# Performance work log

Hardware: AMD Instinct MI355X
Metric: run time of the kernel (lower is better)

## Reference

```python
import jax, jax.numpy as jnp
import numpy as np

N = 50000          # nodes
E_RAND = 800000    # random edges (avg degree 16); self-loops appended per PyG GATConv default
IN = 128
HID = 32
HEADS = 4
OUT = 32
NEG_SLOPE = 0.2    # PyG GATConv default LeakyReLU slope


def setup_inputs() -> dict:
    key = jax.random.key(0)
    ks = jax.random.split(key, 8)
    x = jax.random.normal(ks[0], (N, IN), dtype=jnp.float32)
    src = jax.random.randint(ks[1], (E_RAND,), 0, N)
    dst = jax.random.randint(ks[2], (E_RAND,), 0, N)
    loops = jnp.arange(N)
    src = jnp.concatenate([src, loops])  # [E] with self-loops
    dst = jnp.concatenate([dst, loops])
    inp = {"x": x, "src": src, "dst": dst}
    layer_dims = [(IN, HID), (HID * HEADS, HID), (HID * HEADS, OUT)]
    for l, (din, c) in enumerate(layer_dims):
        k1, k2, k3 = jax.random.split(ks[3 + l], 3)
        s = 1.0 / np.sqrt(din)
        inp[f"W{l}"] = jax.random.uniform(k1, (HEADS * c, din), jnp.float32, -s, s)
        inp[f"asrc{l}"] = jax.random.uniform(k2, (HEADS, c), jnp.float32, -s, s)
        inp[f"adst{l}"] = jax.random.uniform(k3, (HEADS, c), jnp.float32, -s, s)
        inp[f"b{l}"] = jnp.zeros((HEADS * c,), jnp.float32)
    return inp


def _gat_conv(x, src, dst, W, a_src, a_dst, b):
    H, C = a_src.shape
    h = (x @ W.T).reshape(-1, H, C)                     # [N, H, C]
    al_s = jnp.einsum('nhc,hc->nh', h, a_src)           # node-level src score
    al_d = jnp.einsum('nhc,hc->nh', h, a_dst)           # node-level dst score
    e = jax.nn.leaky_relu(al_s[src] + al_d[dst], NEG_SLOPE)  # [E, H]
    # segment softmax over edges sharing the same destination node
    e_max = jax.ops.segment_max(e, dst, num_segments=N)
    e = jnp.exp(e - e_max[dst])
    denom = jax.ops.segment_sum(e, dst, num_segments=N)
    alpha = e / (denom[dst] + 1e-16)                    # [E, H]
    out = jax.ops.segment_sum(alpha[:, :, None] * h[src], dst, num_segments=N)  # [N, H, C]
    return out.reshape(-1, H * C) + b


def reference(x, src, dst, W0, asrc0, adst0, b0, W1, asrc1, adst1, b1, W2, asrc2, adst2, b2):
    params = [(W0, asrc0, adst0, b0), (W1, asrc1, adst1, b1), (W2, asrc2, adst2, b2)]
    h = x
    for i, (W, a_s, a_d, b) in enumerate(params):
        h = _gat_conv(h, src, dst, W, a_s, a_d, b)
        if i != len(params) - 1:
            h = jax.nn.elu(h)  # dropout p=0.5 is identity in eval mode
    return h
```

## Files before the change

kernel.cpp:

```cpp
#include <hip/hip_runtime.h>
#include <stdint.h>

typedef unsigned short ushort_t;
typedef unsigned int uint32;

typedef __attribute__((ext_vector_type(8))) short short8;
typedef __attribute__((ext_vector_type(4))) float floatx4;

#define NEG_SLOPE 0.2f

__device__ __forceinline__ ushort_t f2bf(float f) {
    union { float f; uint32 u; } v; v.f = f;
    uint32 u = v.u;
    uint32 r = (u + 0x7fffu + ((u >> 16) & 1u)) >> 16;
    return (ushort_t)r;
}
__device__ __forceinline__ float2 bf2x(uint32 u) {
    union { uint32 u; float f; } a, b;
    a.u = u << 16; b.u = u & 0xffff0000u;
    float2 r; r.x = a.f; r.y = b.f; return r;
}

__global__ void k_sniff(const uint32* __restrict__ x, int* __restrict__ flag) {
    __shared__ int sh[256];
    int t = threadIdx.x;
    int c = 0;
    for (int i = t; i < 1024; i += 256) {
        uint32 h = x[i] & 0xFFFFu;
        uint32 e = (h >> 7) & 0xFFu;
        if (h == 0u || (e >= 100u && e <= 140u)) c++;
    }
    sh[t] = c; __syncthreads();
    for (int off = 128; off >= 1; off >>= 1) {
        if (t < off) sh[t] += sh[t + off];
        __syncthreads();
    }
    if (t == 0) flag[0] = (sh[0] >= 512) ? 1 : 0;
}

__global__ void k_canon_params(const void* W0, const void* W1, const void* W2,
                               const void* s0, const void* s1, const void* s2,
                               const void* a0, const void* a1, const void* a2,
                               const void* b0, const void* b1, const void* b2,
                               ushort_t* __restrict__ dst, const int* __restrict__ flag) {
    int i = blockIdx.x * 256 + threadIdx.x;
    if (i >= 50304) return;
    const void* src; int off;
    if (i < 49152) {
        int seg = i / 16384; off = i % 16384;
        src = seg == 0 ? W0 : seg == 1 ? W1 : W2;
    } else if (i < 49536) {
        int j = i - 49152; int seg = j / 128; off = j % 128;
        src = seg == 0 ? s0 : seg == 1 ? s1 : s2;
    } else if (i < 49920) {
        int j = i - 49536; int seg = j / 128; off = j % 128;
        src = seg == 0 ? a0 : seg == 1 ? a1 : a2;
    } else {
        int j = i - 49920; int seg = j / 128; off = j % 128;
        src = seg == 0 ? b0 : seg == 1 ? b1 : b2;
    }
    if (flag[0]) dst[i] = ((const ushort_t*)src)[off];
    else         dst[i] = f2bf(((const float*)src)[off]);
}

__global__ void k_hist(const int* __restrict__ dst, int* __restrict__ cnt,
                       int* __restrict__ rank, int E) {
    int e = blockIdx.x * 256 + threadIdx.x;
    if (e < E) rank[e] = atomicAdd(&cnt[dst[e]], 1);
}

__global__ void k_scan_a(const int* __restrict__ cnt, int* __restrict__ ro,
                         int* __restrict__ bsum, int n) {
    __shared__ int sd[256];
    int t = threadIdx.x;
    int base = blockIdx.x * 1024 + t * 4;
    int v0 = (base + 0 < n) ? cnt[base + 0] : 0;
    int v1 = (base + 1 < n) ? cnt[base + 1] : 0;
    int v2 = (base + 2 < n) ? cnt[base + 2] : 0;
    int v3 = (base + 3 < n) ? cnt[base + 3] : 0;
    int s = v0 + v1 + v2 + v3;
    sd[t] = s; __syncthreads();
    for (int off = 1; off < 256; off <<= 1) {
        int x = 0;
        if (t >= off) x = sd[t - off];
        __syncthreads();
        sd[t] += x;
        __syncthreads();
    }
    int run = sd[t] - s;
    run += v0; if (base + 0 < n) ro[base + 1] = run;
    run += v1; if (base + 1 < n) ro[base + 2] = run;
    run += v2; if (base + 2 < n) ro[base + 3] = run;
    run += v3; if (base + 3 < n) ro[base + 4] = run;
    if (t == 255) bsum[blockIdx.x] = sd[255];
}

__global__ void k_scan_bc(int* __restrict__ ro, const int* __restrict__ bsum,
                          int n, int nb) {
    __shared__ int pre[256];
    int t = threadIdx.x;
    if (t == 0) {
        int acc = 0;
        for (int b = 0; b < nb; b++) { pre[b] = acc; acc += bsum[b]; }
    }
    __syncthreads();
    int i = blockIdx.x * 256 + t;
    if (i == 0) ro[0] = 0;
    if (i < n) ro[i + 1] += pre[i >> 10];
}

__global__ void k_scatter(const int* __restrict__ src, const int* __restrict__ dst,
                          const int* __restrict__ ro, const int* __restrict__ rank,
                          int* __restrict__ ssrc, int E) {
    int e = blockIdx.x * 256 + threadIdx.x;
    if (e < E) {
        int d = dst[e];
        ssrc[ro[d] + rank[e]] = src[e] << 8;
    }
}

__global__ __launch_bounds__(256) void k_gemm(const void* __restrict__ actv,
                                              const ushort_t* __restrict__ W,
                                              ushort_t* __restrict__ hb,
                                              float* __restrict__ als,
                                              float* __restrict__ ald,
                                              const ushort_t* __restrict__ asrcp,
                                              const ushort_t* __restrict__ adstp,
                                              int N, int layer0,
                                              const int* __restrict__ flag) {
    int wid = threadIdx.x >> 6, lane = threadIdx.x & 63;
    int n0 = (blockIdx.x * 4 + wid) * 16;
    int mrow = lane & 15, quad = lane >> 4;
    int n = n0 + mrow;
    bool isf32 = (layer0 && !flag[0]);
    short8 a[4];
    if (n < N) {
        if (isf32) {
            const float* ar = (const float*)actv + (size_t)n * 128 + quad * 8;
            #pragma unroll
            for (int kt = 0; kt < 4; kt++) {
                float4 fa = *(const float4*)(ar + kt * 32);
                float4 fb = *(const float4*)(ar + kt * 32 + 4);
                short8 v;
                v[0] = (short)f2bf(fa.x); v[1] = (short)f2bf(fa.y);
                v[2] = (short)f2bf(fa.z); v[3] = (short)f2bf(fa.w);
                v[4] = (short)f2bf(fb.x); v[5] = (short)f2bf(fb.y);
                v[6] = (short)f2bf(fb.z); v[7] = (short)f2bf(fb.w);
                a[kt] = v;
            }
        } else {
            const ushort_t* ar = (const ushort_t*)actv + (size_t)n * 128 + quad * 8;
            #pragma unroll
            for (int kt = 0; kt < 4; kt++) a[kt] = *(const short8*)(ar + kt * 32);
        }
    } else {
        #pragma unroll
        for (int kt = 0; kt < 4; kt++) { short8 z = {0,0,0,0,0,0,0,0}; a[kt] = z; }
    }
    float ps[4], pd[4];
    #pragma unroll
    for (int t = 0; t < 8; t++) {
        if ((t & 1) == 0) {
            #pragma unroll
            for (int r = 0; r < 4; r++) { ps[r] = 0.f; pd[r] = 0.f; }
        }
        const ushort_t* wr = W + (size_t)(t * 16 + mrow) * 128 + quad * 8;
        floatx4 acc = {0.f, 0.f, 0.f, 0.f};
        #pragma unroll
        for (int kt = 0; kt < 4; kt++) {
            short8 b = *(const short8*)(wr + kt * 32);
            acc = __builtin_amdgcn_mfma_f32_16x16x32_bf16(a[kt], b, acc, 0, 0, 0);
        }
        int col = t * 16 + mrow;
        union { uint32 u; float f; } cs, cd;
        cs.u = ((uint32)asrcp[col]) << 16;
        cd.u = ((uint32)adstp[col]) << 16;
        #pragma unroll
        for (int r = 0; r < 4; r++) {
            int rn = n0 + quad * 4 + r;
            if (rn < N) hb[(size_t)rn * 128 + col] = f2bf(acc[r]);
            ps[r] += acc[r] * cs.f;
            pd[r] += acc[r] * cd.f;
        }
        if (t & 1) {
            #pragma unroll
            for (int off = 1; off <= 8; off <<= 1) {
                #pragma unroll
                for (int r = 0; r < 4; r++) {
                    ps[r] += __shfl_xor(ps[r], off);
                    pd[r] += __shfl_xor(pd[r], off);
                }
            }
            int h = t >> 1;
            if (mrow < 8) {
                int r = mrow & 3;
                float vs = r == 0 ? ps[0] : r == 1 ? ps[1] : r == 2 ? ps[2] : ps[3];
                float vd = r == 0 ? pd[0] : r == 1 ? pd[1] : r == 2 ? pd[2] : pd[3];
                int rn = n0 + quad * 4 + r;
                if (rn < N) {
                    float* dp = (mrow < 4) ? als : ald;
                    dp[(size_t)rn * 4 + h] = (mrow < 4) ? vs : vd;
                }
            }
        }
    }
}

__global__ __launch_bounds__(128) void k_agg(const int* __restrict__ ro, const int* __restrict__ ssrc,
                                             const ushort_t* __restrict__ hb,
                                             const float* __restrict__ als, const float* __restrict__ ald_,
                                             const ushort_t* __restrict__ bias,
                                             void* __restrict__ outp, int N, int apply_elu,
                                             int is_final, const int* __restrict__ flag) {
    __shared__ __align__(16) float tsm_all[2][1024];
    __shared__ int osm_all[2][256];
    int wv = threadIdx.x >> 6, lane = threadIdx.x & 63;
    int n = blockIdx.x * 2 + wv;
    if (n >= N) return;
    float* tsm = tsm_all[wv];
    int* osm = osm_all[wv];
    int r0 = ro[n], r1 = ro[n + 1];
    int deg = r1 - r0;
    int degc = deg < 256 ? deg : 256;
    floatx4 ad = *(const floatx4*)(ald_ + (size_t)n * 4);
    const char* alsb = (const char*)als;

    float m0 = -1e30f, m1 = -1e30f, m2 = -1e30f, m3 = -1e30f;
    for (int e = lane; e < degc; e += 64) {
        int off = ssrc[r0 + e];
        osm[e] = off;
        floatx4 as = *(const floatx4*)(alsb + (off >> 4));
        float t0 = as.x + ad.x; t0 = t0 > 0.f ? t0 : NEG_SLOPE * t0; m0 = fmaxf(m0, t0);
        float t1 = as.y + ad.y; t1 = t1 > 0.f ? t1 : NEG_SLOPE * t1; m1 = fmaxf(m1, t1);
        float t2 = as.z + ad.z; t2 = t2 > 0.f ? t2 : NEG_SLOPE * t2; m2 = fmaxf(m2, t2);
        float t3 = as.w + ad.w; t3 = t3 > 0.f ? t3 : NEG_SLOPE * t3; m3 = fmaxf(m3, t3);
        floatx4 t4 = {t0, t1, t2, t3};
        *(floatx4*)(tsm + e * 4) = t4;
    }
    for (int i = r0 + 256 + lane; i < r1; i += 64) {
        int off = ssrc[i];
        floatx4 as = *(const floatx4*)(alsb + (off >> 4));
        float t0 = as.x + ad.x; t0 = t0 > 0.f ? t0 : NEG_SLOPE * t0; m0 = fmaxf(m0, t0);
        float t1 = as.y + ad.y; t1 = t1 > 0.f ? t1 : NEG_SLOPE * t1; m1 = fmaxf(m1, t1);
        float t2 = as.z + ad.z; t2 = t2 > 0.f ? t2 : NEG_SLOPE * t2; m2 = fmaxf(m2, t2);
        float t3 = as.w + ad.w; t3 = t3 > 0.f ? t3 : NEG_SLOPE * t3; m3 = fmaxf(m3, t3);
    }
    #pragma unroll
    for (int off = 32; off >= 1; off >>= 1) {
        m0 = fmaxf(m0, __shfl_xor(m0, off));
        m1 = fmaxf(m1, __shfl_xor(m1, off));
        m2 = fmaxf(m2, __shfl_xor(m2, off));
        m3 = fmaxf(m3, __shfl_xor(m3, off));
    }

    float d0 = 0.f, d1 = 0.f, d2 = 0.f, d3 = 0.f;
    __builtin_amdgcn_wave_barrier();
    for (int e = lane; e < degc; e += 64) {
        floatx4 t4 = *(const floatx4*)(tsm + e * 4);
        float w0 = __expf(t4.x - m0); d0 += w0;
        float w1 = __expf(t4.y - m1); d1 += w1;
        float w2 = __expf(t4.z - m2); d2 += w2;
        float w3 = __expf(t4.w - m3); d3 += w3;
        floatx4 w4 = {w0, w1, w2, w3};
        *(floatx4*)(tsm + e * 4) = w4;
    }
    __builtin_amdgcn_wave_barrier();

    int hd = lane >> 4;
    const char* hbase = (const char*)hb + (lane << 2);
    float a0 = 0.f, a1 = 0.f;
    int j = 0;
    for (; j + 2 <= degc; j += 2) {
        float wa = tsm[j * 4 + hd];
        float wb = tsm[j * 4 + 4 + hd];
        int oa = osm[j], ob = osm[j + 1];
        uint32 ha = *(const uint32*)(hbase + oa);
        uint32 hc = *(const uint32*)(hbase + ob);
        float2 pa = bf2x(ha), pb = bf2x(hc);
        a0 += wa * pa.x; a1 += wa * pa.y;
        a0 += wb * pb.x; a1 += wb * pb.y;
    }
    if (j < degc) {
        float wa = tsm[j * 4 + hd];
        int oa = osm[j];
        uint32 ha = *(const uint32*)(hbase + oa);
        float2 pa = bf2x(ha);
        a0 += wa * pa.x; a1 += wa * pa.y;
    }
    for (int i2 = r0 + 256; i2 < r1; i2++) {
        int off = ssrc[i2];
        floatx4 as = *(const floatx4*)(alsb + (off >> 4));
        float t0 = as.x + ad.x; t0 = t0 > 0.f ? t0 : NEG_SLOPE * t0; float w0 = __expf(t0 - m0);
        float t1 = as.y + ad.y; t1 = t1 > 0.f ? t1 : NEG_SLOPE * t1; float w1 = __expf(t1 - m1);
        float t2 = as.z + ad.z; t2 = t2 > 0.f ? t2 : NEG_SLOPE * t2; float w2 = __expf(t2 - m2);
        float t3 = as.w + ad.w; t3 = t3 > 0.f ? t3 : NEG_SLOPE * t3; float w3 = __expf(t3 - m3);
        if (lane == 0) { d0 += w0; d1 += w1; d2 += w2; d3 += w3; }
        float wsel = hd == 0 ? w0 : hd == 1 ? w1 : hd == 2 ? w2 : w3;
        uint32 ha = *(const uint32*)(hbase + off);
        float2 pa = bf2x(ha);
        a0 += wsel * pa.x; a1 += wsel * pa.y;
    }

    #pragma unroll
    for (int off = 32; off >= 1; off >>= 1) {
        d0 += __shfl_xor(d0, off); d1 += __shfl_xor(d1, off);
        d2 += __shfl_xor(d2, off); d3 += __shfl_xor(d3, off);
    }
    float den = (hd == 0 ? d0 : hd == 1 ? d1 : hd == 2 ? d2 : d3) + 1e-16f;
    float inv = 1.0f / den;
    int c0 = lane * 2;
    float2 bv = bf2x(*(const uint32*)(bias + c0));
    float o0 = a0 * inv + bv.x;
    float o1 = a1 * inv + bv.y;
    if (apply_elu) {
        o0 = o0 > 0.f ? o0 : expm1f(o0);
        o1 = o1 > 0.f ? o1 : expm1f(o1);
    }
    if (is_final && !flag[0]) {
        float2 o; o.x = o0; o.y = o1;
        *(float2*)((float*)outp + (size_t)n * 128 + c0) = o;
    } else {
        uint32 pack = (uint32)f2bf(o0) | ((uint32)f2bf(o1) << 16);
        *(uint32*)((ushort_t*)outp + (size_t)n * 128 + c0) = pack;
    }
}

extern "C" void kernel_launch(void* const* d_in, const int* in_sizes, int n_in,
                              void* d_out, int out_size, void* d_ws, size_t ws_size,
                              hipStream_t stream) {
    const void* x = d_in[0];
    const int* src = (const int*)d_in[1];
    const int* dst = (const int*)d_in[2];
    const int N = in_sizes[0] / 128;
    const int E = in_sizes[1];

    char* p = (char*)d_ws;
    auto alloc = [&](size_t bytes) { char* r = p; p += (bytes + 255) & ~(size_t)255; return r; };
    int*      flag  = (int*)alloc(256);
    int*      ro    = (int*)alloc((size_t)(N + 1) * 4);
    int*      ssrc  = (int*)alloc((size_t)E * 4);
    ushort_t* hb    = (ushort_t*)alloc((size_t)N * 128 * 2);
    float*    als   = (float*)alloc((size_t)N * 4 * 4);
    float*    ald   = (float*)alloc((size_t)N * 4 * 4);
    ushort_t* xact  = (ushort_t*)alloc((size_t)N * 128 * 2);
    ushort_t* pblk  = (ushort_t*)alloc((size_t)50304 * 2);

    int* cnt  = (int*)hb;
    int* bsum = (int*)((char*)hb + (size_t)N * 4);
    int* rank = (int*)xact;

    int g256e = (E + 255) / 256;
    int g256n = (N + 255) / 256;
    int nb = (N + 1023) / 1024;

    k_sniff<<<1, 256, 0, stream>>>((const uint32*)x, flag);
    k_canon_params<<<(50304 + 255) / 256, 256, 0, stream>>>(
        d_in[3], d_in[7], d_in[11],
        d_in[4], d_in[8], d_in[12],
        d_in[5], d_in[9], d_in[13],
        d_in[6], d_in[10], d_in[14],
        pblk, flag);

    hipMemsetAsync(cnt, 0, (size_t)N * 4, stream);
    k_hist<<<g256e, 256, 0, stream>>>(dst, cnt, rank, E);
    k_scan_a<<<nb, 256, 0, stream>>>(cnt, ro, bsum, N);
    k_scan_bc<<<g256n, 256, 0, stream>>>(ro, bsum, N, nb);
    k_scatter<<<g256e, 256, 0, stream>>>(src, dst, ro, rank, ssrc, E);

    int gg = (N + 63) / 64;
    int ga = (N + 1) / 2;
    const void* actin = x;
    for (int l = 0; l < 3; l++) {
        const ushort_t* Wc = pblk + (size_t)l * 16384;
        const ushort_t* As = pblk + 49152 + l * 128;
        const ushort_t* Ad = pblk + 49536 + l * 128;
        const ushort_t* Bc = pblk + 49920 + l * 128;
        void* outp = (l == 2) ? d_out : (void*)xact;
        k_gemm<<<gg, 256, 0, stream>>>(actin, Wc, hb, als, ald, As, Ad, N, l == 0 ? 1 : 0, flag);
        k_agg<<<ga, 128, 0, stream>>>(ro, ssrc, hb, als, ald, Bc, outp, N, l < 2 ? 1 : 0,
                                      l == 2 ? 1 : 0, flag);
        actin = xact;
    }
}
```

Baseline: 382.2 us.

## Fuse setup launches, use 16-bit edge indices, restructure aggregation per wave

Merges parameter canonicalisation with the degree histogram, and the first scan pass with the layer-0 GEMM, so independent work shares one launch. Sorted source indices are now stored as 16-bit values, halving index traffic; this only works while the node count fits in 16 bits. The aggregation kernel now runs one wavefront per node and processes edges in chunks of 64, staging weights and offsets in shared memory. This removes the 256-edge cap and its serial fallback loop, at the cost of recomputing the attention scores in the second pass.

```diff
diff --git a/kernel.cpp b/kernel.cpp
--- a/kernel.cpp
+++ b/kernel.cpp
@@ -38,98 +38,18 @@
     if (t == 0) flag[0] = (sh[0] >= 512) ? 1 : 0;
 }
 
-__global__ void k_canon_params(const void* W0, const void* W1, const void* W2,
-                               const void* s0, const void* s1, const void* s2,
-                               const void* a0, const void* a1, const void* a2,
-                               const void* b0, const void* b1, const void* b2,
-                               ushort_t* __restrict__ dst, const int* __restrict__ flag) {
-    int i = blockIdx.x * 256 + threadIdx.x;
-    if (i >= 50304) return;
-    const void* src; int off;
-    if (i < 49152) {
-        int seg = i / 16384; off = i % 16384;
-        src = seg == 0 ? W0 : seg == 1 ? W1 : W2;
-    } else if (i < 49536) {
-        int j = i - 49152; int seg = j / 128; off = j % 128;
-        src = seg == 0 ? s0 : seg == 1 ? s1 : s2;
-    } else if (i < 49920) {
-        int j = i - 49536; int seg = j / 128; off = j % 128;
-        src = seg == 0 ? a0 : seg == 1 ? a1 : a2;
-    } else {
-        int j = i - 49920; int seg = j / 128; off = j % 128;
-        src = seg == 0 ? b0 : seg == 1 ? b1 : b2;
-    }
-    if (flag[0]) dst[i] = ((const ushort_t*)src)[off];
-    else         dst[i] = f2bf(((const float*)src)[off]);
-}
-
-__global__ void k_hist(const int* __restrict__ dst, int* __restrict__ cnt,
-                       int* __restrict__ rank, int E) {
-    int e = blockIdx.x * 256 + threadIdx.x;
-    if (e < E) rank[e] = atomicAdd(&cnt[dst[e]], 1);
-}
-
-__global__ void k_scan_a(const int* __restrict__ cnt, int* __restrict__ ro,
-                         int* __restrict__ bsum, int n) {
-    __shared__ int sd[256];
-    int t = threadIdx.x;
-    int base = blockIdx.x * 1024 + t * 4;
-    int v0 = (base + 0 < n) ? cnt[base + 0] : 0;
-    int v1 = (base + 1 < n) ? cnt[base + 1] : 0;
-    int v2 = (base + 2 < n) ? cnt[base + 2] : 0;
-    int v3 = (base + 3 < n) ? cnt[base + 3] : 0;
-    int s = v0 + v1 + v2 + v3;
-    sd[t] = s; __syncthreads();
-    for (int off = 1; off < 256; off <<= 1) {
-        int x = 0;
-        if (t >= off) x = sd[t - off];
-        __syncthreads();
-        sd[t] += x;
-        __syncthreads();
-    }
-    int run = sd[t] - s;
-    run += v0; if (base + 0 < n) ro[base + 1] = run;
-    run += v1; if (base + 1 < n) ro[base + 2] = run;
-    run += v2; if (base + 2 < n) ro[base + 3] = run;
-    run += v3; if (base + 3 < n) ro[base + 4] = run;
-    if (t == 255) bsum[blockIdx.x] = sd[255];
-}
-
-__global__ void k_scan_bc(int* __restrict__ ro, const int* __restrict__ bsum,
-                          int n, int nb) {
-    __shared__ int pre[256];
-    int t = threadIdx.x;
-    if (t == 0) {
-        int acc = 0;
-        for (int b = 0; b < nb; b++) { pre[b] = acc; acc += bsum[b]; }
-    }
-    __syncthreads();
-    int i = blockIdx.x * 256 + t;
-    if (i == 0) ro[0] = 0;
-    if (i < n) ro[i + 1] += pre[i >> 10];
-}
-
-__global__ void k_scatter(const int* __restrict__ src, const int* __restrict__ dst,
-                          const int* __restrict__ ro, const int* __restrict__ rank,
-                          int* __restrict__ ssrc, int E) {
-    int e = blockIdx.x * 256 + threadIdx.x;
-    if (e < E) {
-        int d = dst[e];
-        ssrc[ro[d] + rank[e]] = src[e] << 8;
-    }
-}
-
-__global__ __launch_bounds__(256) void k_gemm(const void* __restrict__ actv,
-                                              const ushort_t* __restrict__ W,
-                                              ushort_t* __restrict__ hb,
-                                              float* __restrict__ als,
-                                              float* __restrict__ ald,
-                                              const ushort_t* __restrict__ asrcp,
-                                              const ushort_t* __restrict__ adstp,
-                                              int N, int layer0,
-                                              const int* __restrict__ flag) {
-    int wid = threadIdx.x >> 6, lane = threadIdx.x & 63;
-    int n0 = (blockIdx.x * 4 + wid) * 16;
+__device__ __forceinline__ void gemm_body(int bid, int tid,
+                                          const void* __restrict__ actv,
+                                          const ushort_t* __restrict__ W,
+                                          ushort_t* __restrict__ hb,
+                                          float* __restrict__ als,
+                                          float* __restrict__ ald,
+                                          const ushort_t* __restrict__ asrcp,
+                                          const ushort_t* __restrict__ adstp,
+                                          int N, int layer0,
+                                          const int* __restrict__ flag) {
+    int wid = tid >> 6, lane = tid & 63;
+    int n0 = (bid * 4 + wid) * 16;
     int mrow = lane & 15, quad = lane >> 4;
     int n = n0 + mrow;
     bool isf32 = (layer0 && !flag[0]);
@@ -206,40 +126,128 @@
     }
 }
 
-__global__ __launch_bounds__(128) void k_agg(const int* __restrict__ ro, const int* __restrict__ ssrc,
-                                             const ushort_t* __restrict__ hb,
-                                             const float* __restrict__ als, const float* __restrict__ ald_,
-                                             const ushort_t* __restrict__ bias,
-                                             void* __restrict__ outp, int N, int apply_elu,
-                                             int is_final, const int* __restrict__ flag) {
-    __shared__ __align__(16) float tsm_all[2][1024];
-    __shared__ int osm_all[2][256];
-    int wv = threadIdx.x >> 6, lane = threadIdx.x & 63;
-    int n = blockIdx.x * 2 + wv;
-    if (n >= N) return;
-    float* tsm = tsm_all[wv];
-    int* osm = osm_all[wv];
+__global__ __launch_bounds__(256) void k_gemm(const void* __restrict__ actv,
+                                              const ushort_t* __restrict__ W,
+                                              ushort_t* __restrict__ hb,
+                                              float* __restrict__ als,
+                                              float* __restrict__ ald,
+                                              const ushort_t* __restrict__ asrcp,
+                                              const ushort_t* __restrict__ adstp,
+                                              int N, const int* __restrict__ flag) {
+    gemm_body(blockIdx.x, threadIdx.x, actv, W, hb, als, ald, asrcp, adstp, N, 0, flag);
+}
+
+__global__ void k_f1(const void* W0, const void* W1, const void* W2,
+                     const void* s0, const void* s1, const void* s2,
+                     const void* a0, const void* a1, const void* a2,
+                     const void* b0, const void* b1, const void* b2,
+                     ushort_t* __restrict__ pblk, const int* __restrict__ flag,
+                     const int* __restrict__ dst, int* __restrict__ cnt,
+                     int* __restrict__ rank, int E) {
+    if (blockIdx.x < 197) {
+        int i = blockIdx.x * 256 + threadIdx.x;
+        if (i >= 50304) return;
+        const void* src; int off;
+        if (i < 49152) {
+            int seg = i / 16384; off = i % 16384;
+            src = seg == 0 ? W0 : seg == 1 ? W1 : W2;
+        } else if (i < 49536) {
+            int j = i - 49152; int seg = j / 128; off = j % 128;
+            src = seg == 0 ? s0 : seg == 1 ? s1 : s2;
+        } else if (i < 49920) {
+            int j = i - 49536; int seg = j / 128; off = j % 128;
+            src = seg == 0 ? a0 : seg == 1 ? a1 : a2;
+        } else {
+            int j = i - 49920; int seg = j / 128; off = j % 128;
+            src = seg == 0 ? b0 : seg == 1 ? b1 : b2;
+        }
+        if (flag[0]) pblk[i] = ((const ushort_t*)src)[off];
+        else         pblk[i] = f2bf(((const float*)src)[off]);
+    } else {
+        int e = (blockIdx.x - 197) * 256 + threadIdx.x;
+        if (e < E) rank[e] = atomicAdd(&cnt[dst[e]], 1);
+    }
+}
+
+__global__ __launch_bounds__(256) void k_f2(const int* __restrict__ cnt, int* __restrict__ ro,
+                                            int* __restrict__ bsum, int n, int nb,
+                                            const void* __restrict__ actv,
+                                            const ushort_t* __restrict__ W,
+                                            ushort_t* __restrict__ hb,
+                                            float* __restrict__ als, float* __restrict__ ald,
+                                            const ushort_t* __restrict__ asrcp,
+                                            const ushort_t* __restrict__ adstp,
+                                            int N, const int* __restrict__ flag) {
+    if ((int)blockIdx.x < nb) {
+        __shared__ int sd[256];
+        int t = threadIdx.x;
+        int base = blockIdx.x * 1024 + t * 4;
+        int v0 = (base + 0 < n) ? cnt[base + 0] : 0;
+        int v1 = (base + 1 < n) ? cnt[base + 1] : 0;
+        int v2 = (base + 2 < n) ? cnt[base + 2] : 0;
+        int v3 = (base + 3 < n) ? cnt[base + 3] : 0;
+        int s = v0 + v1 + v2 + v3;
+        sd[t] = s; __syncthreads();
+        for (int off = 1; off < 256; off <<= 1) {
+            int x = 0;
+            if (t >= off) x = sd[t - off];
+            __syncthreads();
+            sd[t] += x;
+            __syncthreads();
+        }
+        int run = sd[t] - s;
+        run += v0; if (base + 0 < n) ro[base + 1] = run;
+        run += v1; if (base + 1 < n) ro[base + 2] = run;
+        run += v2; if (base + 2 < n) ro[base + 3] = run;
+        run += v3; if (base + 3 < n) ro[base + 4] = run;
+        if (t == 255) bsum[blockIdx.x] = sd[255];
+    } else {
+        gemm_body(blockIdx.x - nb, threadIdx.x, actv, W, hb, als, ald, asrcp, adstp, N, 1, flag);
+    }
+}
+
+__global__ void k_scan_bc(int* __restrict__ ro, const int* __restrict__ bsum,
+                          int n, int nb) {
+    __shared__ int pre[256];
+    int t = threadIdx.x;
+    if (t == 0) {
+        int acc = 0;
+        for (int b = 0; b < nb; b++) { pre[b] = acc; acc += bsum[b]; }
+    }
+    __syncthreads();
+    int i = blockIdx.x * 256 + t;
+    if (i == 0) ro[0] = 0;
+    if (i < n) ro[i + 1] += pre[i >> 10];
+}
+
+__global__ void k_scatter(const int* __restrict__ src, const int* __restrict__ dst,
+                          const int* __restrict__ ro, const int* __restrict__ rank,
+                          ushort_t* __restrict__ ssrc, int E) {
+    int e = blockIdx.x * 256 + threadIdx.x;
+    if (e < E) {
+        int d = dst[e];
+        ssrc[ro[d] + rank[e]] = (ushort_t)src[e];
+    }
+}
+
+__global__ __launch_bounds__(64) void k_agg(const int* __restrict__ ro,
+                                            const ushort_t* __restrict__ ssrc,
+                                            const ushort_t* __restrict__ hb,
+                                            const float* __restrict__ als,
+                                            const float* __restrict__ ald_,
+                                            const ushort_t* __restrict__ bias,
+                                            void* __restrict__ outp, int N, int apply_elu,
+                                            int is_final, const int* __restrict__ flag) {
+    int n = blockIdx.x;
+    int lane = threadIdx.x;
     int r0 = ro[n], r1 = ro[n + 1];
-    int deg = r1 - r0;
-    int degc = deg < 256 ? deg : 256;
     floatx4 ad = *(const floatx4*)(ald_ + (size_t)n * 4);
     const char* alsb = (const char*)als;
 
     float m0 = -1e30f, m1 = -1e30f, m2 = -1e30f, m3 = -1e30f;
-    for (int e = lane; e < degc; e += 64) {
-        int off = ssrc[r0 + e];
-        osm[e] = off;
-        floatx4 as = *(const floatx4*)(alsb + (off >> 4));
-        float t0 = as.x + ad.x; t0 = t0 > 0.f ? t0 : NEG_SLOPE * t0; m0 = fmaxf(m0, t0);
-        float t1 = as.y + ad.y; t1 = t1 > 0.f ? t1 : NEG_SLOPE * t1; m1 = fmaxf(m1, t1);
-        float t2 = as.z + ad.z; t2 = t2 > 0.f ? t2 : NEG_SLOPE * t2; m2 = fmaxf(m2, t2);
-        float t3 = as.w + ad.w; t3 = t3 > 0.f ? t3 : NEG_SLOPE * t3; m3 = fmaxf(m3, t3);
-        floatx4 t4 = {t0, t1, t2, t3};
-        *(floatx4*)(tsm + e * 4) = t4;
-    }
-    for (int i = r0 + 256 + lane; i < r1; i += 64) {
-        int off = ssrc[i];
-        floatx4 as = *(const floatx4*)(alsb + (off >> 4));
+    for (int i = r0 + lane; i < r1; i += 64) {
+        int s = ssrc[i];
+        floatx4 as = *(const floatx4*)(alsb + (s << 4));
         float t0 = as.x + ad.x; t0 = t0 > 0.f ? t0 : NEG_SLOPE * t0; m0 = fmaxf(m0, t0);
         float t1 = as.y + ad.y; t1 = t1 > 0.f ? t1 : NEG_SLOPE * t1; m1 = fmaxf(m1, t1);
         float t2 = as.z + ad.z; t2 = t2 > 0.f ? t2 : NEG_SLOPE * t2; m2 = fmaxf(m2, t2);
@@ -253,54 +261,37 @@
         m3 = fmaxf(m3, __shfl_xor(m3, off));
     }
 
+    __shared__ __align__(16) float wsm[256];
+    __shared__ int osm[64];
+    float a0 = 0.f, a1 = 0.f;
     float d0 = 0.f, d1 = 0.f, d2 = 0.f, d3 = 0.f;
-    __builtin_amdgcn_wave_barrier();
-    for (int e = lane; e < degc; e += 64) {
-        floatx4 t4 = *(const floatx4*)(tsm + e * 4);
-        float w0 = __expf(t4.x - m0); d0 += w0;
-        float w1 = __expf(t4.y - m1); d1 += w1;
-        float w2 = __expf(t4.z - m2); d2 += w2;
-        float w3 = __expf(t4.w - m3); d3 += w3;
-        floatx4 w4 = {w0, w1, w2, w3};
-        *(floatx4*)(tsm + e * 4) = w4;
-    }
-    __builtin_amdgcn_wave_barrier();
-
     int hd = lane >> 4;
-    const char* hbase = (const char*)hb + (lane << 2);
-    float a0 = 0.f, a1 = 0.f;
-    int j = 0;
-    for (; j + 2 <= degc; j += 2) {
-        float wa = tsm[j * 4 + hd];
-        float wb = tsm[j * 4 + 4 + hd];
-        int oa = osm[j], ob = osm[j + 1];
-        uint32 ha = *(const uint32*)(hbase + oa);
-        uint32 hc = *(const uint32*)(hbase + ob);
-        float2 pa = bf2x(ha), pb = bf2x(hc);
-        a0 += wa * pa.x; a1 += wa * pa.y;
-        a0 += wb * pb.x; a1 += wb * pb.y;
-    }
-    if (j < degc) {
-        float wa = tsm[j * 4 + hd];
-        int oa = osm[j];
-        uint32 ha = *(const uint32*)(hbase + oa);
-        float2 pa = bf2x(ha);
-        a0 += wa * pa.x; a1 += wa * pa.y;
-    }
-    for (int i2 = r0 + 256; i2 < r1; i2++) {
-        int off = ssrc[i2];
-        floatx4 as = *(const floatx4*)(alsb + (off >> 4));
-        float t0 = as.x + ad.x; t0 = t0 > 0.f ? t0 : NEG_SLOPE * t0; float w0 = __expf(t0 - m0);
-        float t1 = as.y + ad.y; t1 = t1 > 0.f ? t1 : NEG_SLOPE * t1; float w1 = __expf(t1 - m1);
-        float t2 = as.z + ad.z; t2 = t2 > 0.f ? t2 : NEG_SLOPE * t2; float w2 = __expf(t2 - m2);
-        float t3 = as.w + ad.w; t3 = t3 > 0.f ? t3 : NEG_SLOPE * t3; float w3 = __expf(t3 - m3);
-        if (lane == 0) { d0 += w0; d1 += w1; d2 += w2; d3 += w3; }
-        float wsel = hd == 0 ? w0 : hd == 1 ? w1 : hd == 2 ? w2 : w3;
-        uint32 ha = *(const uint32*)(hbase + off);
-        float2 pa = bf2x(ha);
-        a0 += wsel * pa.x; a1 += wsel * pa.y;
-    }
-
+    int laneb = lane << 2;
+    for (int base = r0; base < r1; base += 64) {
+        int i = base + lane;
+        if (i < r1) {
+            int s = ssrc[i];
+            floatx4 as = *(const floatx4*)(alsb + (s << 4));
+            float t0 = as.x + ad.x; t0 = t0 > 0.f ? t0 : NEG_SLOPE * t0; float w0 = __expf(t0 - m0); d0 += w0;
+            float t1 = as.y + ad.y; t1 = t1 > 0.f ? t1 : NEG_SLOPE * t1; float w1 = __expf(t1 - m1); d1 += w1;
+            float t2 = as.z + ad.z; t2 = t2 > 0.f ? t2 : NEG_SLOPE * t2; float w2 = __expf(t2 - m2); d2 += w2;
+            float t3 = as.w + ad.w; t3 = t3 > 0.f ? t3 : NEG_SLOPE * t3; float w3 = __expf(t3 - m3); d3 += w3;
+            osm[lane] = s << 8;
+            floatx4 w4 = {w0, w1, w2, w3};
+            *(floatx4*)(wsm + lane * 4) = w4;
+        }
+        __builtin_amdgcn_wave_barrier();
+        int cend = min(64, r1 - base);
+        #pragma unroll 4
+        for (int j = 0; j < cend; j++) {
+            float wj = wsm[j * 4 + hd];
+            uint32 h2 = *(const uint32*)((const char*)hb + (uint32)(osm[j] + laneb));
+            float2 p = bf2x(h2);
+            a0 += wj * p.x;
+            a1 += wj * p.y;
+        }
+        __builtin_amdgcn_wave_barrier();
+    }
     #pragma unroll
     for (int off = 32; off >= 1; off >>= 1) {
         d0 += __shfl_xor(d0, off); d1 += __shfl_xor(d1, off);
@@ -337,48 +328,46 @@
     char* p = (char*)d_ws;
     auto alloc = [&](size_t bytes) { char* r = p; p += (bytes + 255) & ~(size_t)255; return r; };
     int*      flag  = (int*)alloc(256);
+    int*      bsum  = (int*)alloc(256 * 4);
     int*      ro    = (int*)alloc((size_t)(N + 1) * 4);
-    int*      ssrc  = (int*)alloc((size_t)E * 4);
+    ushort_t* ssrc  = (ushort_t*)alloc((size_t)E * 2);
     ushort_t* hb    = (ushort_t*)alloc((size_t)N * 128 * 2);
     float*    als   = (float*)alloc((size_t)N * 4 * 4);
     float*    ald   = (float*)alloc((size_t)N * 4 * 4);
     ushort_t* xact  = (ushort_t*)alloc((size_t)N * 128 * 2);
     ushort_t* pblk  = (ushort_t*)alloc((size_t)50304 * 2);
 
-    int* cnt  = (int*)hb;
-    int* bsum = (int*)((char*)hb + (size_t)N * 4);
+    int* cnt  = (int*)ssrc;
     int* rank = (int*)xact;
 
     int g256e = (E + 255) / 256;
     int g256n = (N + 255) / 256;
     int nb = (N + 1023) / 1024;
+    int gg = (N + 63) / 64;
 
     k_sniff<<<1, 256, 0, stream>>>((const uint32*)x, flag);
-    k_canon_params<<<(50304 + 255) / 256, 256, 0, stream>>>(
+    hipMemsetAsync(cnt, 0, (size_t)N * 4, stream);
+    k_f1<<<197 + g256e, 256, 0, stream>>>(
         d_in[3], d_in[7], d_in[11],
         d_in[4], d_in[8], d_in[12],
         d_in[5], d_in[9], d_in[13],
         d_in[6], d_in[10], d_in[14],
-        pblk, flag);
-
-    hipMemsetAsync(cnt, 0, (size_t)N * 4, stream);
-    k_hist<<<g256e, 256, 0, stream>>>(dst, cnt, rank, E);
-    k_scan_a<<<nb, 256, 0, stream>>>(cnt, ro, bsum, N);
+        pblk, flag, dst, cnt, rank, E);
+    k_f2<<<nb + gg, 256, 0, stream>>>(cnt, ro, bsum, N, nb,
+        x, pblk, hb, als, ald, pblk + 49152, pblk + 49536, N, flag);
     k_scan_bc<<<g256n, 256, 0, stream>>>(ro, bsum, N, nb);
     k_scatter<<<g256e, 256, 0, stream>>>(src, dst, ro, rank, ssrc, E);
 
-    int gg = (N + 63) / 64;
-    int ga = (N + 1) / 2;
-    const void* actin = x;
     for (int l = 0; l < 3; l++) {
-        const ushort_t* Wc = pblk + (size_t)l * 16384;
         const ushort_t* As = pblk + 49152 + l * 128;
         const ushort_t* Ad = pblk + 49536 + l * 128;
         const ushort_t* Bc = pblk + 49920 + l * 128;
         void* outp = (l == 2) ? d_out : (void*)xact;
-        k_gemm<<<gg, 256, 0, stream>>>(actin, Wc, hb, als, ald, As, Ad, N, l == 0 ? 1 : 0, flag);
-        k_agg<<<ga, 128, 0, stream>>>(ro, ssrc, hb, als, ald, Bc, outp, N, l < 2 ? 1 : 0,
-                                      l == 2 ? 1 : 0, flag);
-        actin = xact;
-    }
-}
+        if (l > 0) {
+            const ushort_t* Wc = pblk + (size_t)l * 16384;
+            k_gemm<<<gg, 256, 0, stream>>>(xact, Wc, hb, als, ald, As, Ad, N, flag);
+        }
+        k_agg<<<N, 64, 0, stream>>>(ro, ssrc, hb, als, ald, Bc, outp, N, l < 2 ? 1 : 0,
+                                    l == 2 ? 1 : 0, flag);
+    }
+}
```

Result: faster. 351.2 us (-8.1%).
